# Optimization experiments

Measured on AMD Instinct MI355X. Metric: run time of the kernel, lower is better.

## Reference

```python
import jax, jax.numpy as jnp
import numpy as np
import math

B, C_LOW, C_HIGH, H, W = 8, 128, 256, 128, 128
KS = 7

def _conv(x, w, b, pad):
    out = jax.lax.conv_general_dilated(
        x, w, window_strides=(1, 1), padding=[(pad, pad), (pad, pad)],
        dimension_numbers=('NCHW', 'OIHW', 'NCHW'))
    return out + b[None, :, None, None]

def setup_inputs() -> dict:
    key = jax.random.key(0)
    ks = jax.random.split(key, 6)
    def he(k, shape):  # matches torch init: normal(0, sqrt(2/(kh*kw*out)))
        n = shape[2] * shape[3] * shape[0]
        return jax.random.normal(k, shape, jnp.float32) * math.sqrt(2.0 / n)
    return {
        'cur_low': jax.random.normal(ks[0], (B, C_LOW, H, W), jnp.float32),
        'key_low': jax.random.normal(ks[1], (B, C_LOW, H, W), jnp.float32),
        'key_high': jax.random.normal(ks[2], (B, C_HIGH, H, W), jnp.float32),
        'w_red': he(ks[3], (256, C_LOW, 3, 3)),
        'b_red': jnp.zeros((256,), jnp.float32),
        'w2': he(ks[4], (256, 512, 3, 3)),
        'b2': jnp.zeros((256,), jnp.float32),
        'w3': he(ks[5], (KS * KS, 256, 1, 1)),
        'b3': jnp.zeros((KS * KS,), jnp.float32),
    }

def reference(cur_low, key_low, key_high, w_red, b_red, w2, b2, w3, b3):
    # KernelWeightPredictor
    cur = jax.nn.relu(_conv(cur_low, w_red, b_red, 1))
    key = jax.nn.relu(_conv(key_low, w_red, b_red, 1))
    x = jax.nn.relu(_conv(jnp.concatenate([cur, key], axis=1), w2, b2, 1))
    x = jax.nn.relu(_conv(x, w3, b3, 0))            # [B, k*k, H, W]
    x = jax.nn.softmax(x, axis=1)
    b, k2, h, w = x.shape
    kernels = jnp.transpose(x, (0, 2, 3, 1)).reshape(b, h, w, KS, KS)
    # SpatiallyVariantConvolution: per-pixel 7x7 kernel applied to key_high
    pad = KS // 2
    fp = jnp.pad(key_high, ((0, 0), (0, 0), (pad, pad), (pad, pad)))
    out = jnp.zeros_like(key_high)
    for i in range(KS):          # fixed 49-iteration unrolled loop; avoids
        for j in range(KS):      # materializing the [B,C,H,W,K,K] patch tensor
            out = out + fp[:, :, i:i + h, j:j + w] * kernels[:, None, :, :, i, j]
    return out
```

## Files before the change

### kernel.cpp

```cpp
#include <hip/hip_runtime.h>
#include <stdint.h>
#include <stddef.h>

#define BN   8
#define HN   128
#define WN   128
#define HP   130
#define CLOW 128
#define CMID 256
#define KO   49

#define KHB_H 134
#define KHB_W 144
#define KHB_PLANE (KHB_H * KHB_W)

typedef __attribute__((ext_vector_type(4))) float f32x4;
typedef __attribute__((ext_vector_type(8))) short bf16x8;

typedef __attribute__((address_space(1))) const uint8_t ga_u8;
typedef __attribute__((address_space(3))) uint8_t lds_u8;

__device__ __forceinline__ short f2bf(float f) {
    uint32_t u = __float_as_uint(f);
    u += 0x7fffu + ((u >> 16) & 1u);
    return (short)(u >> 16);
}
__device__ __forceinline__ float bf2f(short s) {
    return __uint_as_float(((uint32_t)(uint16_t)s) << 16);
}
__device__ __forceinline__ void gload16(const void* g, void* l) {
    __builtin_amdgcn_global_load_lds((ga_u8*)g, (lds_u8*)l, 16, 0, 0);
}

__global__ __launch_bounds__(256) void zero_border_all_kernel(
    short* __restrict__ b0, short* __restrict__ b1,
    short* __restrict__ b2, short* __restrict__ b3) {
    const int which = blockIdx.y;
    short* buf = (which == 0) ? b0 : (which == 1) ? b1 : (which == 2) ? b2 : b3;
    const int gsh = (which < 2) ? 4 : 5;
    const int C = (which < 2) ? 128 : 256;
    int t = blockIdx.x * 256 + threadIdx.x;
    int cell = t >> gsh, g = t & ((1 << gsh) - 1);
    if (cell >= 8 * 516) return;
    int b = cell / 516, r = cell - b * 516;
    int y, x;
    if (r < 260) { y = (r >= 130) ? 129 : 0; x = (r >= 130) ? (r - 130) : r; }
    else { int j = r - 260; y = 1 + (j >> 1); x = (j & 1) ? 129 : 0; }
    uint4 z = {0u, 0u, 0u, 0u};
    *(uint4*)&buf[(((size_t)b * HP + y) * HP + x) * C + g * 8] = z;
}

__global__ __launch_bounds__(256) void convert_pad_kernel(
    const float* __restrict__ src0, const float* __restrict__ src1,
    short* __restrict__ dst0, short* __restrict__ dst1) {
    __shared__ short t[128 * 132];
    const int tid = threadIdx.x;
    const int by = blockIdx.x;
    const int b = by >> 7, y = by & 127;
    const float* src = blockIdx.y ? src1 : src0;
    short* dst = blockIdx.y ? dst1 : dst0;
    for (int k = 0; k < 64; ++k) {
        int i = (k << 8) + tid;
        int c = i >> 7, x = i & 127;
        t[x * 132 + c] = f2bf(src[(((size_t)b * CLOW + c) * HN + y) * WN + x]);
    }
    __syncthreads();
    short* drow = dst + (((size_t)b * HP + (y + 1)) * HP + 1) * CLOW;
    for (int k = 0; k < 64; ++k) {
        int i = (k << 8) + tid;
        int x = i >> 7, c = i & 127;
        drow[x * CLOW + c] = t[x * 132 + c];
    }
}

__global__ __launch_bounds__(256) void pack_w_all_kernel(
    const float* __restrict__ w1, short* __restrict__ wp1,
    const float* __restrict__ w2, short* __restrict__ wp2,
    const float* __restrict__ w3, short* __restrict__ wp3) {
    int i = blockIdx.x * 256 + threadIdx.x;
    if (i < 256 * 1152 + 256 * 4608) {
        const float* w; short* wp; int CIN, K;
        if (i < 256 * 1152) { w = w1; wp = wp1; CIN = 128; K = 1152; }
        else { i -= 256 * 1152; w = w2; wp = wp2; CIN = 512; K = 4608; }
        int cout = i / K;
        int r = i - cout * K;
        int t = r >> 6;
        int j = r & 63;
        int cb = t / 9;
        int tap = t - cb * 9;
        int cin = cb * 64 + j;
        wp[i] = f2bf(w[((size_t)cout * CIN + cin) * 9 + tap]);
    } else {
        int j = i - (256 * 1152 + 256 * 4608);
        if (j >= 64 * 256) return;
        int o = j >> 8, ch = j & 255;
        wp3[j] = (o < KO) ? f2bf(w3[o * 256 + ch]) : (short)0;
    }
}

template <int CIN, bool OPAD, bool FUSE>
__global__ __launch_bounds__(512, 2) void conv_8ph_kernel(
    const short* __restrict__ in_a, const short* __restrict__ in_b,
    const short* __restrict__ wp, const float* __restrict__ bias,
    short* __restrict__ out_a, short* __restrict__ out_b,
    const short* __restrict__ w3p, const float* __restrict__ b3,
    float* __restrict__ z) {
    constexpr int K = 9 * CIN;
    constexpr int NT = K / 64;
    constexpr bool DUAL = (CIN == 512);
    constexpr int PST = DUAL ? 256 : CIN;
    extern __shared__ __align__(16) short lds[];
    const int tid = threadIdx.x;
    int bx = blockIdx.x;
    bx = (bx & 7) * 64 + (bx >> 3);
    const int b = bx >> 6, y0 = (bx & 63) << 1;
    const short* inA = DUAL ? in_a : (blockIdx.z ? in_b : in_a);
    const short* inB = DUAL ? in_b : inA;
    short* out = (!DUAL && blockIdx.z) ? out_b : out_a;

    const int lane = tid & 63, wv = tid >> 6;
    const int wm = wv >> 2, wn = wv & 3;
    const int lr = lane & 15, lk = lane >> 4;

    const int rA = tid >> 3, cc = tid & 7;
    const int cs = cc ^ (rA & 7);
    const int pthrA0 = rA * PST + cs * 8;
    const int pthrA1 = (rA + 64) * PST + cs * 8;
    const int pthrB0 = rA * K + cs * 8;
    const int pthrB1 = (rA + 64) * K + cs * 8;
    const int dA0 = rA * 64 + cc * 8;
    const int dB0 = rA * 64 + cc * 8;

    const int arow = (wm * 128 + lr) * 64;
    const int brow = (wn * 64 + lr) * 64;
    const int cof0 = ((lk) ^ (lr & 7)) * 8;
    const int cof1 = ((4 + lk) ^ (lr & 7)) * 8;

    f32x4 acc[8][4];
    f32x4 zero = {0.f, 0.f, 0.f, 0.f};
    #pragma unroll
    for (int i = 0; i < 8; ++i)
        #pragma unroll
        for (int j = 0; j < 4; ++j) acc[i][j] = zero;

    auto STAGE2 = [&](int t2, int which, short* bufA, short* bufB) {
        const int cb = (t2 * 57) >> 9;
        const int tap = t2 - cb * 9;
        const int ch0v = cb << 6;
        const short* src = (!DUAL || ch0v < 256) ? inA : inB;
        const int ch0 = DUAL ? (ch0v & 255) : ch0v;
        const int ky = (tap * 11) >> 5;
        const int kx = tap - ky * 3;
        if (which == 0 || which == 2) {
            const int po = (which == 0) ? pthrA0 : pthrA1;
            const int doff = (which == 0) ? 0 : 64 * 64;
            const short* s0 = src + ((size_t)(b * HP + (y0 + ky)) * HP + kx) * PST + ch0;
            gload16(s0 + po, bufA + doff + dA0);
            gload16(s0 + (HP * PST) + po, bufA + 128 * 64 + doff + dA0);
        } else {
            const int h2 = (which == 1) ? 0 : 1;
            const short* sb = wp + (size_t)(h2 * 128) * K + t2 * 64;
            short* d = bufB + h2 * 128 * 64 + dB0;
            gload16(sb + pthrB0, d);
            gload16(sb + pthrB1, d + 64 * 64);
        }
    };

    auto LDA = [&](const short* bufA, int mh, bf16x8 (&a)[4][2]) {
        #pragma unroll
        for (int i = 0; i < 4; ++i) {
            const int ro = arow + (mh * 64 + i * 16) * 64;
            a[i][0] = *(const bf16x8*)(bufA + ro + cof0);
            a[i][1] = *(const bf16x8*)(bufA + ro + cof1);
        }
    };
    auto LDB = [&](const short* bufB, int nh, bf16x8 (&bb)[2][2]) {
        #pragma unroll
        for (int j = 0; j < 2; ++j) {
            const int ro = brow + (nh * 32 + j * 16) * 64;
            bb[j][0] = *(const bf16x8*)(bufB + ro + cof0);
            bb[j][1] = *(const bf16x8*)(bufB + ro + cof1);
        }
    };

#define PH_PRE() do { __builtin_amdgcn_sched_barrier(0); \
                      __builtin_amdgcn_s_barrier(); \
                      asm volatile("s_waitcnt lgkmcnt(0)" ::: "memory"); \
                      __builtin_amdgcn_sched_barrier(0); \
                      __builtin_amdgcn_s_setprio(1); } while (0)
#define PH_POST() do { __builtin_amdgcn_s_setprio(0); \
                       __builtin_amdgcn_sched_barrier(0); \
                       __builtin_amdgcn_s_barrier(); } while (0)
#define MFMA_Q(A_, B_, MH, NH) do { \
    _Pragma("unroll") \
    for (int i_ = 0; i_ < 4; ++i_) { \
        _Pragma("unroll") \
        for (int j_ = 0; j_ < 2; ++j_) { \
            acc[(MH)*4+i_][(NH)*2+j_] = __builtin_amdgcn_mfma_f32_16x16x32_bf16( \
                A_[i_][0], B_[j_][0], acc[(MH)*4+i_][(NH)*2+j_], 0, 0, 0); \
            acc[(MH)*4+i_][(NH)*2+j_] = __builtin_amdgcn_mfma_f32_16x16x32_bf16( \
                A_[i_][1], B_[j_][1], acc[(MH)*4+i_][(NH)*2+j_], 0, 0, 0); \
        } \
    } } while (0)

    short* const A0 = lds;
    short* const A1 = lds + 16384;
    short* const B0 = lds + 32768;
    short* const B1 = lds + 49152;

    STAGE2(0, 0, A0, B0); STAGE2(0, 1, A0, B0);
    STAGE2(0, 2, A0, B0); STAGE2(0, 3, A0, B0);
    STAGE2(1, 0, A1, B1); STAGE2(1, 1, A1, B1);
    STAGE2(1, 2, A1, B1); STAGE2(1, 3, A1, B1);
    asm volatile("s_waitcnt vmcnt(8)" ::: "memory");
    __builtin_amdgcn_sched_barrier(0);
    __builtin_amdgcn_s_barrier();

    auto TILE = [&](int t, short* bufA, short* bufB) {
        const int t2 = t + 2;
        const bool st = (t2 < NT);
        bf16x8 ar[4][2], br0[2][2], br1[2][2];
        LDA(bufA, 0, ar);
        LDB(bufB, 0, br0);
        if (st) STAGE2(t2, 0, bufA, bufB);
        PH_PRE();
        MFMA_Q(ar, br0, 0, 0);
        PH_POST();
        LDB(bufB, 1, br1);
        if (st) STAGE2(t2, 1, bufA, bufB);
        PH_PRE();
        MFMA_Q(ar, br1, 0, 1);
        PH_POST();
        LDA(bufA, 1, ar);
        if (st) STAGE2(t2, 2, bufA, bufB);
        PH_PRE();
        MFMA_Q(ar, br0, 1, 0);
        PH_POST();
        if (st) STAGE2(t2, 3, bufA, bufB);
        PH_PRE();
        MFMA_Q(ar, br1, 1, 1);
        __builtin_amdgcn_s_setprio(0);
        __builtin_amdgcn_sched_barrier(0);
        if (st)                asm volatile("s_waitcnt vmcnt(8)" ::: "memory");
        else if (t == NT - 2)  asm volatile("s_waitcnt vmcnt(0)" ::: "memory");
        __builtin_amdgcn_sched_barrier(0);
        __builtin_amdgcn_s_barrier();
    };

    for (int t = 0; t < NT; t += 2) {
        TILE(t,     A0, B0);
        TILE(t + 1, A1, B1);
    }
#undef PH_PRE
#undef PH_POST
#undef MFMA_Q

    float bvs[4];
    #pragma unroll
    for (int nf = 0; nf < 4; ++nf) bvs[nf] = bias[wn * 64 + nf * 16 + lr];

    if constexpr (!FUSE) {
        #pragma unroll
        for (int mf = 0; mf < 8; ++mf) {
            #pragma unroll
            for (int rr = 0; rr < 4; ++rr) {
                const int p = wm * 128 + mf * 16 + lk * 4 + rr;
                const int y = y0 + (p >> 7), x = p & 127;
                short* op;
                if (OPAD)
                    op = out + ((size_t)(b * HP + (y + 1)) * HP + (x + 1)) * CMID + wn * 64 + lr;
                else
                    op = out + ((size_t)((b * HN + y) * WN + x)) * CMID + wn * 64 + lr;
                #pragma unroll
                for (int nf = 0; nf < 4; ++nf)
                    op[nf * 16] = f2bf(fmaxf(acc[mf][nf][rr] + bvs[nf], 0.f));
            }
        }
    } else {
        short* const Xh  = lds;
        short* const W3s = lds + 32768;

        #pragma unroll
        for (int sweep = 0; sweep < 4; ++sweep) {
            const int s = sweep * 512 + tid;
            const int o = s >> 5, c = s & 31;
            gload16(w3p + o * 256 + ((c ^ (o & 7)) << 3), W3s + s * 8);
        }

        const int oo = wn * 16 + lr;
        const float b3v = (oo < KO) ? b3[oo] : 0.f;

        #pragma unroll 1
        for (int r = 0; r < 2; ++r) {
            if (wm == r) {
                #pragma unroll
                for (int nf = 0; nf < 4; ++nf) {
                    const int ch = wn * 64 + nf * 16 + lr;
                    const int ck = ch >> 3, el = ch & 7;
                    #pragma unroll
                    for (int mf = 0; mf < 8; ++mf) {
                        #pragma unroll
                        for (int rr = 0; rr < 4; ++rr) {
                            const int px = mf * 16 + lk * 4 + rr;
                            Xh[px * 256 + ((ck ^ (px & 7)) << 3) + el] =
                                f2bf(fmaxf(acc[mf][nf][rr] + bvs[nf], 0.f));
                        }
                    }
                }
            }
            __syncthreads();
            f32x4 a2[4];
            #pragma unroll
            for (int m = 0; m < 4; ++m) {
                a2[m][0] = b3v; a2[m][1] = b3v; a2[m][2] = b3v; a2[m][3] = b3v;
            }
            #pragma unroll
            for (int ks = 0; ks < 8; ++ks) {
                const bf16x8 bfr =
                    *(const bf16x8*)&W3s[oo * 256 + (((ks * 4 + lk) ^ (oo & 7)) << 3)];
                #pragma unroll
                for (int m = 0; m < 4; ++m) {
                    const int px = wm * 64 + m * 16 + lr;
                    const bf16x8 afr =
                        *(const bf16x8*)&Xh[px * 256 + (((ks * 4 + lk) ^ (px & 7)) << 3)];
                    a2[m] = __builtin_amdgcn_mfma_f32_16x16x32_bf16(afr, bfr, a2[m], 0, 0, 0);
                }
            }
            float* zp = z + ((size_t)(b * 16384 + (y0 + r) * 128)) * 64;
            #pragma unroll
            for (int m = 0; m < 4; ++m) {
                #pragma unroll
                for (int r2 = 0; r2 < 4; ++r2) {
                    const int px = wm * 64 + m * 16 + lk * 4 + r2;
                    zp[px * 64 + oo] = a2[m][r2];
                }
            }
            if (r == 0) __syncthreads();
        }
    }
}

__global__ __launch_bounds__(256) void softmax3_kernel(
    const float* __restrict__ z, float* __restrict__ attn) {
    const int p = blockIdx.x * 256 + threadIdx.x;
    const int b = p >> 14, hw = p & 16383;
    const float* zp = z + (size_t)p * 64;
    float zz[KO];
    #pragma unroll
    for (int q = 0; q < 12; ++q) {
        f32x4 v = *(const f32x4*)&zp[q * 4];
        zz[q * 4 + 0] = fmaxf(v[0], 0.f);
        zz[q * 4 + 1] = fmaxf(v[1], 0.f);
        zz[q * 4 + 2] = fmaxf(v[2], 0.f);
        zz[q * 4 + 3] = fmaxf(v[3], 0.f);
    }
    zz[48] = fmaxf(zp[48], 0.f);
    float m = zz[0];
    #pragma unroll
    for (int o = 1; o < KO; ++o) m = fmaxf(m, zz[o]);
    float s = 0.f;
    #pragma unroll
    for (int o = 0; o < KO; ++o) { float e = __expf(zz[o] - m); zz[o] = e; s += e; }
    const float inv = 1.f / s;
    float* ap = attn + (((size_t)b * KO) << 14) + hw;
    #pragma unroll
    for (int o = 0; o < KO; ++o) ap[(size_t)o << 14] = zz[o] * inv;
}

__global__ __launch_bounds__(256) void pad_kh_kernel(
    const float* __restrict__ kh, short* __restrict__ khb) {
    const int bc = blockIdx.x;
    const float* src = kh + (size_t)bc * (HN * WN);
    short* dst = khb + (size_t)bc * KHB_PLANE;
    for (int i = threadIdx.x; i < KHB_H * (KHB_W / 8); i += 256) {
        int yy = i / (KHB_W / 8);
        int g = i - yy * (KHB_W / 8);
        int ys = yy - 3;
        bf16x8 v;
        #pragma unroll
        for (int t = 0; t < 8; ++t) {
            int xs = g * 8 + t - 4;
            float f = 0.f;
            if ((unsigned)ys < 128u && (unsigned)xs < 128u) f = src[(ys << 7) + xs];
            v[t] = f2bf(f);
        }
        *(bf16x8*)&dst[yy * KHB_W + g * 8] = v;
    }
}

__global__ __launch_bounds__(256) void svc3_kernel(
    const short* __restrict__ khb, const float* __restrict__ attn,
    float* __restrict__ out) {
    __shared__ float a_s[KO * 64];
    const int tid = threadIdx.x;
    int by = blockIdx.y;
    by = (by & 7) * 128 + (by >> 3);
    const int b = by >> 7, y = by & 127;
    const int x0 = blockIdx.x * 64;

    for (int i = tid; i < KO * 64; i += 256) {
        int o = i >> 6, px = i & 63;
        a_s[i] = attn[(((size_t)b * KO + o) << 14) + (y << 7) + x0 + px];
    }
    __syncthreads();

    const int ci = tid >> 3;
    const int pg = tid & 7;
    const int p0 = x0 + pg * 8;

    float acc[8][8];
    #pragma unroll
    for (int c = 0; c < 8; ++c)
        #pragma unroll
        for (int j = 0; j < 8; ++j) acc[c][j] = 0.f;

    const short* kbase = khb + (((size_t)b * 256 + ci) * KHB_H + y) * KHB_W + p0;

    #pragma unroll 1
    for (int dy = 0; dy < 7; ++dy) {
        f32x4 av[14];
        #pragma unroll
        for (int dx = 0; dx < 7; ++dx) {
            av[dx * 2]     = *(const f32x4*)&a_s[(dy * 7 + dx) * 64 + pg * 8];
            av[dx * 2 + 1] = *(const f32x4*)&a_s[(dy * 7 + dx) * 64 + pg * 8 + 4];
        }
        const short* krow = kbase + dy * KHB_W;
        #pragma unroll
        for (int c = 0; c < 8; ++c) {
            const short* kp = krow + (size_t)c * 32 * KHB_PLANE;
            bf16x8 k0 = *(const bf16x8*)(kp);
            bf16x8 k1 = *(const bf16x8*)(kp + 8);
            float win[16];
            #pragma unroll
            for (int t = 0; t < 8; ++t) { win[t] = bf2f(k0[t]); win[t + 8] = bf2f(k1[t]); }
            #pragma unroll
            for (int dx = 0; dx < 7; ++dx) {
                #pragma unroll
                for (int j = 0; j < 8; ++j)
                    acc[c][j] = fmaf(win[j + dx + 1], av[dx * 2 + (j >> 2)][j & 3],
                                     acc[c][j]);
            }
        }
    }

    #pragma unroll
    for (int c = 0; c < 8; ++c) {
        float* op = out + (((size_t)b * 256 + ci + c * 32) << 14) + (y << 7) + p0;
        f32x4 r0 = {acc[c][0], acc[c][1], acc[c][2], acc[c][3]};
        f32x4 r1 = {acc[c][4], acc[c][5], acc[c][6], acc[c][7]};
        *(f32x4*)op = r0;
        *(f32x4*)(op + 4) = r1;
    }
}

extern "C" void kernel_launch(void* const* d_in, const int* in_sizes, int n_in,
                              void* d_out, int out_size, void* d_ws, size_t ws_size,
                              hipStream_t stream) {
    (void)in_sizes; (void)n_in; (void)out_size; (void)ws_size;
    const float* cur_low  = (const float*)d_in[0];
    const float* key_low  = (const float*)d_in[1];
    const float* key_high = (const float*)d_in[2];
    const float* w_red    = (const float*)d_in[3];
    const float* b_red    = (const float*)d_in[4];
    const float* w2       = (const float*)d_in[5];
    const float* b2       = (const float*)d_in[6];
    const float* w3       = (const float*)d_in[7];
    const float* b3       = (const float*)d_in[8];
    float* out = (float*)d_out;
    char* ws = (char*)d_ws;

    const size_t SZ_ATTN = (size_t)BN * KO * HN * WN * 4;
    const size_t SZ_XPAD = (size_t)BN * HP * HP * CLOW * 2;
    const size_t SZ_YPAD = (size_t)BN * HP * HP * CMID * 2;
    float* attn  = (float*)(ws);
    short* xpadc = (short*)(ws + SZ_ATTN);
    short* xpadk = (short*)(ws + SZ_ATTN + SZ_XPAD);
    float* z     = (float*)(ws + SZ_ATTN);
    short* khb   = (short*)(ws + SZ_ATTN);
    short* ypadc = (short*)(ws + SZ_ATTN + 2 * SZ_XPAD);
    short* ypadk = (short*)(ws + SZ_ATTN + 2 * SZ_XPAD + SZ_YPAD);
    short* w1p   = (short*)(ws + SZ_ATTN + 2 * SZ_XPAD + 2 * SZ_YPAD);
    short* w2p   = (short*)((char*)w1p + (size_t)256 * 1152 * 2);
    short* w3p   = (short*)((char*)d_out + (size_t)134217728 - 32768);

    hipFuncSetAttribute((const void*)conv_8ph_kernel<128, true, false>,
                        hipFuncAttributeMaxDynamicSharedMemorySize, 131072);
    hipFuncSetAttribute((const void*)conv_8ph_kernel<512, false, true>,
                        hipFuncAttributeMaxDynamicSharedMemorySize, 131072);

    zero_border_all_kernel<<<dim3(516, 4), 256, 0, stream>>>(xpadc, xpadk, ypadc, ypadk);
    convert_pad_kernel<<<dim3(1024, 2), 256, 0, stream>>>(cur_low, key_low, xpadc, xpadk);
    pack_w_all_kernel<<<(256 * (1152 + 4608) + 64 * 256 + 255) / 256, 256, 0, stream>>>(
        w_red, w1p, w2, w2p, w3, w3p);

    conv_8ph_kernel<128, true, false><<<dim3(512, 1, 2), 512, 131072, stream>>>(
        xpadc, xpadk, w1p, b_red, ypadc, ypadk, nullptr, nullptr, nullptr);

    conv_8ph_kernel<512, false, true><<<dim3(512, 1, 1), 512, 131072, stream>>>(
        ypadc, ypadk, w2p, b2, nullptr, nullptr, w3p, b3, z);

    softmax3_kernel<<<512, 256, 0, stream>>>(z, attn);

    pad_kh_kernel<<<2048, 256, 0, stream>>>(key_high, khb);
    svc3_kernel<<<dim3(2, 1024), 256, 0, stream>>>(khb, attn, out);
}
```

Baseline: 675.5 us.

## Fuse softmax into spatially-variant conv and vectorize input conversion

Removes the standalone softmax kernel and the attn buffer. The SVC kernel now reads the 64-wide logits directly and computes relu+softmax with four lanes per pixel and shuffle reductions. The input convert/pad kernel switches to float4 loads and 16-byte stores with a padded LDS stride. The conv pipeline issues the second B fragment load earlier with a partial lgkmcnt wait. Workspace is reorganized so z and khb alias dead buffers.

```diff
diff --git a/kernel.cpp b/kernel.cpp
--- a/kernel.cpp
+++ b/kernel.cpp
@@ -53,23 +53,27 @@
 __global__ __launch_bounds__(256) void convert_pad_kernel(
     const float* __restrict__ src0, const float* __restrict__ src1,
     short* __restrict__ dst0, short* __restrict__ dst1) {
-    __shared__ short t[128 * 132];
+    __shared__ short t[128 * 136];
     const int tid = threadIdx.x;
     const int by = blockIdx.x;
     const int b = by >> 7, y = by & 127;
     const float* src = blockIdx.y ? src1 : src0;
     short* dst = blockIdx.y ? dst1 : dst0;
-    for (int k = 0; k < 64; ++k) {
-        int i = (k << 8) + tid;
-        int c = i >> 7, x = i & 127;
-        t[x * 132 + c] = f2bf(src[(((size_t)b * CLOW + c) * HN + y) * WN + x]);
+    #pragma unroll
+    for (int k = 0; k < 16; ++k) {
+        int slot = k * 256 + tid;
+        int c = slot >> 5, xg = slot & 31;
+        f32x4 v = *(const f32x4*)&src[(((size_t)b * CLOW + c) * HN + y) * WN + xg * 4];
+        #pragma unroll
+        for (int j = 0; j < 4; ++j) t[(xg * 4 + j) * 136 + c] = f2bf(v[j]);
     }
     __syncthreads();
     short* drow = dst + (((size_t)b * HP + (y + 1)) * HP + 1) * CLOW;
-    for (int k = 0; k < 64; ++k) {
-        int i = (k << 8) + tid;
-        int x = i >> 7, c = i & 127;
-        drow[x * CLOW + c] = t[x * 132 + c];
+    #pragma unroll
+    for (int k = 0; k < 8; ++k) {
+        int slot = k * 256 + tid;
+        int x = slot >> 4, cg = slot & 15;
+        *(bf16x8*)&drow[x * CLOW + cg * 8] = *(const bf16x8*)&t[x * 136 + cg * 8];
     }
 }
 
@@ -183,6 +187,11 @@
         }
     };
 
+#define PH_PRE4() do { __builtin_amdgcn_sched_barrier(0); \
+                       __builtin_amdgcn_s_barrier(); \
+                       asm volatile("s_waitcnt lgkmcnt(4)" ::: "memory"); \
+                       __builtin_amdgcn_sched_barrier(0); \
+                       __builtin_amdgcn_s_setprio(1); } while (0)
 #define PH_PRE() do { __builtin_amdgcn_sched_barrier(0); \
                       __builtin_amdgcn_s_barrier(); \
                       asm volatile("s_waitcnt lgkmcnt(0)" ::: "memory"); \
@@ -222,11 +231,11 @@
         bf16x8 ar[4][2], br0[2][2], br1[2][2];
         LDA(bufA, 0, ar);
         LDB(bufB, 0, br0);
+        LDB(bufB, 1, br1);
         if (st) STAGE2(t2, 0, bufA, bufB);
-        PH_PRE();
+        PH_PRE4();
         MFMA_Q(ar, br0, 0, 0);
         PH_POST();
-        LDB(bufB, 1, br1);
         if (st) STAGE2(t2, 1, bufA, bufB);
         PH_PRE();
         MFMA_Q(ar, br1, 0, 1);
@@ -251,6 +260,7 @@
         TILE(t,     A0, B0);
         TILE(t + 1, A1, B1);
     }
+#undef PH_PRE4
 #undef PH_PRE
 #undef PH_POST
 #undef MFMA_Q
@@ -340,33 +350,6 @@
     }
 }
 
-__global__ __launch_bounds__(256) void softmax3_kernel(
-    const float* __restrict__ z, float* __restrict__ attn) {
-    const int p = blockIdx.x * 256 + threadIdx.x;
-    const int b = p >> 14, hw = p & 16383;
-    const float* zp = z + (size_t)p * 64;
-    float zz[KO];
-    #pragma unroll
-    for (int q = 0; q < 12; ++q) {
-        f32x4 v = *(const f32x4*)&zp[q * 4];
-        zz[q * 4 + 0] = fmaxf(v[0], 0.f);
-        zz[q * 4 + 1] = fmaxf(v[1], 0.f);
-        zz[q * 4 + 2] = fmaxf(v[2], 0.f);
-        zz[q * 4 + 3] = fmaxf(v[3], 0.f);
-    }
-    zz[48] = fmaxf(zp[48], 0.f);
-    float m = zz[0];
-    #pragma unroll
-    for (int o = 1; o < KO; ++o) m = fmaxf(m, zz[o]);
-    float s = 0.f;
-    #pragma unroll
-    for (int o = 0; o < KO; ++o) { float e = __expf(zz[o] - m); zz[o] = e; s += e; }
-    const float inv = 1.f / s;
-    float* ap = attn + (((size_t)b * KO) << 14) + hw;
-    #pragma unroll
-    for (int o = 0; o < KO; ++o) ap[(size_t)o << 14] = zz[o] * inv;
-}
-
 __global__ __launch_bounds__(256) void pad_kh_kernel(
     const float* __restrict__ kh, short* __restrict__ khb) {
     const int bc = blockIdx.x;
@@ -388,8 +371,8 @@
     }
 }
 
-__global__ __launch_bounds__(256) void svc3_kernel(
-    const short* __restrict__ khb, const float* __restrict__ attn,
+__global__ __launch_bounds__(256) void svc4_kernel(
+    const float* __restrict__ z, const short* __restrict__ khb,
     float* __restrict__ out) {
     __shared__ float a_s[KO * 64];
     const int tid = threadIdx.x;
@@ -398,9 +381,36 @@
     const int b = by >> 7, y = by & 127;
     const int x0 = blockIdx.x * 64;
 
-    for (int i = tid; i < KO * 64; i += 256) {
-        int o = i >> 6, px = i & 63;
-        a_s[i] = attn[(((size_t)b * KO + o) << 14) + (y << 7) + x0 + px];
+    {
+        const int px = tid >> 2, l = tid & 3;
+        const float* zp = z + ((size_t)(b * 16384 + (y << 7) + x0 + px)) * 64 + l * 16;
+        float v[16];
+        #pragma unroll
+        for (int q = 0; q < 4; ++q) {
+            f32x4 t4 = *(const f32x4*)&zp[q * 4];
+            v[q * 4 + 0] = fmaxf(t4[0], 0.f);
+            v[q * 4 + 1] = fmaxf(t4[1], 0.f);
+            v[q * 4 + 2] = fmaxf(t4[2], 0.f);
+            v[q * 4 + 3] = fmaxf(t4[3], 0.f);
+        }
+        #pragma unroll
+        for (int j = 1; j < 16; ++j) if (l == 3) v[j] = -1e30f;
+        float m = v[0];
+        #pragma unroll
+        for (int j = 1; j < 16; ++j) m = fmaxf(m, v[j]);
+        m = fmaxf(m, __shfl_xor(m, 1, 64));
+        m = fmaxf(m, __shfl_xor(m, 2, 64));
+        float s = 0.f;
+        #pragma unroll
+        for (int j = 0; j < 16; ++j) { v[j] = __expf(v[j] - m); s += v[j]; }
+        s += __shfl_xor(s, 1, 64);
+        s += __shfl_xor(s, 2, 64);
+        const float inv = 1.f / s;
+        #pragma unroll
+        for (int j = 0; j < 16; ++j) {
+            const int o = l * 16 + j;
+            if (o < KO) a_s[o * 64 + px] = v[j] * inv;
+        }
     }
     __syncthreads();
 
@@ -469,18 +479,16 @@
     float* out = (float*)d_out;
     char* ws = (char*)d_ws;
 
-    const size_t SZ_ATTN = (size_t)BN * KO * HN * WN * 4;
     const size_t SZ_XPAD = (size_t)BN * HP * HP * CLOW * 2;
     const size_t SZ_YPAD = (size_t)BN * HP * HP * CMID * 2;
-    float* attn  = (float*)(ws);
-    short* xpadc = (short*)(ws + SZ_ATTN);
-    short* xpadk = (short*)(ws + SZ_ATTN + SZ_XPAD);
-    float* z     = (float*)(ws + SZ_ATTN);
-    short* khb   = (short*)(ws + SZ_ATTN);
-    short* ypadc = (short*)(ws + SZ_ATTN + 2 * SZ_XPAD);
-    short* ypadk = (short*)(ws + SZ_ATTN + 2 * SZ_XPAD + SZ_YPAD);
-    short* w1p   = (short*)(ws + SZ_ATTN + 2 * SZ_XPAD + 2 * SZ_YPAD);
-    short* w2p   = (short*)((char*)w1p + (size_t)256 * 1152 * 2);
+    short* xpadc = (short*)(ws);
+    short* xpadk = (short*)(ws + SZ_XPAD);
+    short* ypadc = (short*)(ws + 2 * SZ_XPAD);
+    short* ypadk = (short*)(ws + 2 * SZ_XPAD + SZ_YPAD);
+    short* w1p   = (short*)(ws + 2 * SZ_XPAD + 2 * SZ_YPAD);
+    short* w2p   = w1p + (size_t)256 * 1152;
+    float* z     = (float*)(ws);
+    short* khb   = (short*)(ws + 2 * SZ_XPAD);
     short* w3p   = (short*)((char*)d_out + (size_t)134217728 - 32768);
 
     hipFuncSetAttribute((const void*)conv_8ph_kernel<128, true, false>,
@@ -499,8 +507,6 @@
     conv_8ph_kernel<512, false, true><<<dim3(512, 1, 1), 512, 131072, stream>>>(
         ypadc, ypadk, w2p, b2, nullptr, nullptr, w3p, b3, z);
 
-    softmax3_kernel<<<512, 256, 0, stream>>>(z, attn);
-
     pad_kh_kernel<<<2048, 256, 0, stream>>>(key_high, khb);
-    svc3_kernel<<<dim3(2, 1024), 256, 0, stream>>>(khb, attn, out);
-}
+    svc4_kernel<<<dim3(2, 1024), 256, 0, stream>>>(z, khb, out);
+}
```

Result: faster. 654.5 us (-3.1%).
